# Performance work log

Hardware: AMD Instinct MI355X
Metric: run time of the kernel (lower is better)

## Reference

```python
import jax, jax.numpy as jnp
import numpy as np

B, S, D = 8, 2048, 1024
NEG_INF = jnp.float32(-1e30)  # stand-in for -inf; rows with all-masked are overwritten anyway


def setup_inputs() -> dict:
    key = jax.random.key(0)
    ks = jax.random.split(key, 10)
    query = jax.random.normal(ks[0], (B, S, D), dtype=jnp.float32)
    key_t = jax.random.normal(ks[1], (B, S, D), dtype=jnp.float32)
    value = jax.random.normal(ks[2], (B, S, D), dtype=jnp.float32)
    # pad mask: prefix of valid tokens per batch element (realistic ragged batch)
    lengths = jax.random.randint(ks[3], (B,), S // 2, S + 1)
    pad_masks = jnp.arange(S)[None, :] < lengths[:, None]  # (B, S) bool
    # causal mask, same lower-triangular pattern per batch element
    causal = jnp.tril(jnp.ones((S, S), dtype=bool))
    causal_masks = jnp.broadcast_to(causal, (B, S, S))
    # Linear params (torch nn.Linear: y = x @ W.T + b)
    scale = 0.02
    Wq = jax.random.normal(ks[4], (D, D), dtype=jnp.float32) * scale
    bq = jnp.zeros((D,), dtype=jnp.float32)
    Wk = jax.random.normal(ks[5], (D, D), dtype=jnp.float32) * scale
    bk = jnp.zeros((D,), dtype=jnp.float32)
    Wv = jax.random.normal(ks[6], (D, D), dtype=jnp.float32) * scale
    bv = jnp.zeros((D,), dtype=jnp.float32)
    return {"query": query, "key": key_t, "value": value,
            "pad_masks": pad_masks, "causal_masks": causal_masks,
            "Wq": Wq, "bq": bq, "Wk": Wk, "bk": bk, "Wv": Wv, "bv": bv}


def reference(query, key, value, pad_masks, causal_masks, Wq, bq, Wk, bk, Wv, bv):
    d_model = query.shape[-1]
    Q = jnp.einsum('bsd,ed->bse', query, Wq) + bq
    K = jnp.einsum('bsd,ed->bse', key, Wk) + bk
    V = jnp.einsum('bsd,ed->bse', value, Wv) + bv
    scores = jnp.einsum('bqd,bkd->bqk', Q, K) / jnp.sqrt(jnp.float32(d_model))
    combined = pad_masks[:, None, :] & causal_masks              # (B, S, S)
    row_any = jnp.any(combined, axis=-1, keepdims=True)          # (B, S, 1)
    scores = jnp.where(combined, scores, NEG_INF)
    scores = jnp.where(row_any, scores, jnp.zeros_like(scores))
    attn = jax.nn.softmax(scores, axis=-1)
    attn = jnp.where(row_any, attn, jnp.zeros_like(attn))
    # multiply by pad mask along the QUERY axis (faithful to the torch transpose)
    attn = attn * pad_masks[:, :, None].astype(attn.dtype)
    seq_emds = jnp.einsum('bqk,bkd->bqd', attn, V)
    return seq_emds, attn
```

## Files before the change

### kernel.cpp

```cpp
#include <hip/hip_runtime.h>
#include <hip/hip_bf16.h>

#define B_ 8
#define S_ 2048
#define D_ 1024
#define SCALE 0.03125f

typedef __attribute__((ext_vector_type(4))) float f32x4;
typedef __attribute__((ext_vector_type(8))) short short8;
typedef __attribute__((ext_vector_type(4))) short short4v;

static __device__ inline unsigned short f2bf(float f) {
    unsigned int u = __float_as_uint(f);
    u += 0x7FFF + ((u >> 16) & 1);
    return (unsigned short)(u >> 16);
}

static __device__ __forceinline__ void gload16(const void* g, void* l) {
    __builtin_amdgcn_global_load_lds(
        (const __attribute__((address_space(1))) unsigned int*)g,
        (__attribute__((address_space(3))) unsigned int*)l, 16, 0, 0);
}

static __device__ __forceinline__ void pipe_sync() {
    asm volatile("s_waitcnt vmcnt(0)" ::: "memory");
    __builtin_amdgcn_s_barrier();
    __builtin_amdgcn_sched_barrier(0);
}

static __device__ __forceinline__ int xcd_swz(int hw, int nwg) {
    return (hw & 7) * (nwg >> 3) + (hw >> 3);
}

__global__ void lengths_kernel(const unsigned char* __restrict__ pm, int* __restrict__ lens) {
    __shared__ int cnt[B_];
    int tid = threadIdx.x;
    if (tid < B_) cnt[tid] = 0;
    __syncthreads();
    int layout;
    if (pm[0] == 1 && pm[1] == 1) layout = 0;
    else if (pm[0] == 1) layout = 1;
    else layout = 2;
    for (int i = tid; i < B_ * S_; i += blockDim.x) {
        bool v;
        if (layout == 0) v = pm[i] != 0;
        else if (layout == 1) v = ((const int*)pm)[i] != 0;
        else v = ((const float*)pm)[i] != 0.0f;
        if (v) atomicAdd(&cnt[i >> 11], 1);
    }
    __syncthreads();
    if (tid < B_) lens[tid] = cnt[tid];
}

__global__ void convert_all_kernel(const float* __restrict__ q, const float* __restrict__ k,
                                   const float* __restrict__ v,
                                   const float* __restrict__ Wq, const float* __restrict__ Wk,
                                   const float* __restrict__ Wv,
                                   unsigned short* __restrict__ Xb,
                                   unsigned short* __restrict__ Wb) {
    const int z = blockIdx.z;
    const float* src;
    unsigned short* dst;
    int n;
    if (z < 3) {
        src = (z == 0) ? q : (z == 1) ? k : v;
        dst = Xb + (size_t)z * B_ * S_ * D_;
        n = B_ * S_ * D_;
    } else {
        src = (z == 3) ? Wq : (z == 4) ? Wk : Wv;
        dst = Wb + (size_t)(z - 3) * D_ * D_;
        n = D_ * D_;
    }
    int idx = (blockIdx.x * 256 + threadIdx.x) * 8;
    if (idx >= n) return;
    float4 a = *(const float4*)(src + idx);
    float4 b = *(const float4*)(src + idx + 4);
    short8 o;
    o[0] = (short)f2bf(a.x); o[1] = (short)f2bf(a.y);
    o[2] = (short)f2bf(a.z); o[3] = (short)f2bf(a.w);
    o[4] = (short)f2bf(b.x); o[5] = (short)f2bf(b.y);
    o[6] = (short)f2bf(b.z); o[7] = (short)f2bf(b.w);
    *(short8*)(dst + idx) = o;
}

__global__ void proj_bf16_kernel(const unsigned short* __restrict__ Xb3,
                                 const unsigned short* __restrict__ Wb3,
                                 const float* __restrict__ bq, const float* __restrict__ bk,
                                 const float* __restrict__ bv,
                                 unsigned short* __restrict__ Qb,
                                 unsigned short* __restrict__ Kb,
                                 unsigned short* __restrict__ Vt) {
    const int log_id = xcd_swz(blockIdx.x, 3 * (B_ * S_ / 128) * (D_ / 128));
    const int z = log_id >> 10;
    const int rem = log_id & 1023;
    const int m0 = (rem >> 3) * 128;
    const int n0 = (rem & 7) * 128;

    const unsigned short* Xb = Xb3 + (size_t)z * B_ * S_ * D_;
    const unsigned short* Wb = Wb3 + (size_t)z * D_ * D_;
    const float* bias = (z == 0) ? bq : (z == 1) ? bk : bv;

    __shared__ unsigned short As[2][128 * 32];
    __shared__ unsigned short Bs[2][128 * 32];

    const int tid = threadIdx.x;
    const int lane = tid & 63, w = tid >> 6;
    const int wr = w >> 1, wc = w & 1;
    const int g = lane >> 4, l15 = lane & 15;

    const int flat0 = (w * 2 + 0) * 1024 + lane * 16;
    const int flat1 = (w * 2 + 1) * 1024 + lane * 16;
    const int r0 = flat0 >> 6, cb0 = flat0 & 63;
    const int r1 = flat1 >> 6, cb1 = flat1 & 63;

    auto stage = [&](int buf, int kk) {
        gload16((const char*)Xb + ((size_t)(m0 + r0) * D_ + kk) * 2 + cb0, (char*)&As[buf][0] + flat0);
        gload16((const char*)Xb + ((size_t)(m0 + r1) * D_ + kk) * 2 + cb1, (char*)&As[buf][0] + flat1);
        gload16((const char*)Wb + ((size_t)(n0 + r0) * D_ + kk) * 2 + cb0, (char*)&Bs[buf][0] + flat0);
        gload16((const char*)Wb + ((size_t)(n0 + r1) * D_ + kk) * 2 + cb1, (char*)&Bs[buf][0] + flat1);
    };

    f32x4 acc[4][4];
    const f32x4 z4 = {0.f, 0.f, 0.f, 0.f};
    for (int a = 0; a < 4; ++a)
        for (int b2 = 0; b2 < 4; ++b2) acc[a][b2] = z4;

    stage(0, 0);
    pipe_sync();
    int cur = 0;
    for (int kk = 0; kk < D_; kk += 32) {
        if (kk + 32 < D_) stage(cur ^ 1, kk + 32);
        short8 a_frag[4], b_frag[4];
#pragma unroll
        for (int mf = 0; mf < 4; ++mf)
            a_frag[mf] = *(const short8*)(&As[cur][(wr * 64 + mf * 16 + l15) * 32 + g * 8]);
#pragma unroll
        for (int nf = 0; nf < 4; ++nf)
            b_frag[nf] = *(const short8*)(&Bs[cur][(wc * 64 + nf * 16 + l15) * 32 + g * 8]);
        __builtin_amdgcn_s_setprio(1);
#pragma unroll
        for (int mf = 0; mf < 4; ++mf)
#pragma unroll
            for (int nf = 0; nf < 4; ++nf)
                acc[mf][nf] = __builtin_amdgcn_mfma_f32_16x16x32_bf16(a_frag[mf], b_frag[nf], acc[mf][nf], 0, 0, 0);
        __builtin_amdgcn_s_setprio(0);
        pipe_sync();
        cur ^= 1;
    }

    if (z < 2) {
        unsigned short* O = (z == 0) ? Qb : Kb;
#pragma unroll
        for (int mf = 0; mf < 4; ++mf) {
#pragma unroll
            for (int nf = 0; nf < 4; ++nf) {
                int gm = m0 + wr * 64 + mf * 16 + 4 * g;
                int gn = n0 + wc * 64 + nf * 16 + l15;
                float bb = bias[gn];
#pragma unroll
                for (int i = 0; i < 4; ++i)
                    O[(size_t)(gm + i) * D_ + gn] = f2bf(acc[mf][nf][i] + bb);
            }
        }
    } else {
#pragma unroll
        for (int mf = 0; mf < 4; ++mf) {
#pragma unroll
            for (int nf = 0; nf < 4; ++nf) {
                int gm = m0 + wr * 64 + mf * 16 + 4 * g;
                int b = gm >> 11, tok = gm & 2047;
                int gn = n0 + wc * 64 + nf * 16 + l15;
                float bb = bias[gn];
                short4v sv;
#pragma unroll
                for (int i = 0; i < 4; ++i) sv[i] = (short)f2bf(acc[mf][nf][i] + bb);
                *(short4v*)(&Vt[((size_t)b * D_ + gn) * S_ + tok]) = sv;
            }
        }
    }
}

__global__ void proj_kernel(const float* __restrict__ q, const float* __restrict__ k,
                            const float* __restrict__ v,
                            const float* __restrict__ Wq, const float* __restrict__ Wk,
                            const float* __restrict__ Wv,
                            const float* __restrict__ bq, const float* __restrict__ bk,
                            const float* __restrict__ bv,
                            unsigned short* __restrict__ Qb, unsigned short* __restrict__ Kb,
                            unsigned short* __restrict__ Vt) {
    const int z = blockIdx.z;
    const float* X = (z == 0) ? q : (z == 1) ? k : v;
    const float* W = (z == 0) ? Wq : (z == 1) ? Wk : Wv;
    const float* bias = (z == 0) ? bq : (z == 1) ? bk : bv;

    __shared__ short As[128 * 40];
    __shared__ short Bs[128 * 40];

    const int m0 = blockIdx.y * 128;
    const int n0 = blockIdx.x * 128;
    const int tid = threadIdx.x;
    const int lane = tid & 63, wid = tid >> 6;
    const int wr = wid >> 1, wc = wid & 1;
    const int g = lane >> 4, l15 = lane & 15;

    f32x4 acc[4][4];
    const f32x4 z4 = {0.f, 0.f, 0.f, 0.f};
    for (int a = 0; a < 4; ++a)
        for (int b2 = 0; b2 < 4; ++b2) acc[a][b2] = z4;

    for (int kk = 0; kk < D_; kk += 32) {
#pragma unroll
        for (int it = 0; it < 4; ++it) {
            int flat = it * 1024 + tid * 4;
            int r = flat >> 5, c = flat & 31;
            float4 va = *(const float4*)(X + (size_t)(m0 + r) * D_ + kk + c);
            short4v sa = {(short)f2bf(va.x), (short)f2bf(va.y), (short)f2bf(va.z), (short)f2bf(va.w)};
            *(short4v*)(&As[r * 40 + c]) = sa;
            float4 vb = *(const float4*)(W + (size_t)(n0 + r) * D_ + kk + c);
            short4v sb = {(short)f2bf(vb.x), (short)f2bf(vb.y), (short)f2bf(vb.z), (short)f2bf(vb.w)};
            *(short4v*)(&Bs[r * 40 + c]) = sb;
        }
        __syncthreads();
        short8 a_frag[4], b_frag[4];
#pragma unroll
        for (int mf = 0; mf < 4; ++mf)
            a_frag[mf] = *(const short8*)(&As[(wr * 64 + mf * 16 + l15) * 40 + g * 8]);
#pragma unroll
        for (int nf = 0; nf < 4; ++nf)
            b_frag[nf] = *(const short8*)(&Bs[(wc * 64 + nf * 16 + l15) * 40 + g * 8]);
#pragma unroll
        for (int mf = 0; mf < 4; ++mf)
#pragma unroll
            for (int nf = 0; nf < 4; ++nf)
                acc[mf][nf] = __builtin_amdgcn_mfma_f32_16x16x32_bf16(a_frag[mf], b_frag[nf], acc[mf][nf], 0, 0, 0);
        __syncthreads();
    }

    if (z < 2) {
        unsigned short* O = (z == 0) ? Qb : Kb;
#pragma unroll
        for (int mf = 0; mf < 4; ++mf) {
#pragma unroll
            for (int nf = 0; nf < 4; ++nf) {
                int gm = m0 + wr * 64 + mf * 16 + 4 * g;
                int gn = n0 + wc * 64 + nf * 16 + l15;
                float bb = bias[gn];
#pragma unroll
                for (int i = 0; i < 4; ++i)
                    O[(size_t)(gm + i) * D_ + gn] = f2bf(acc[mf][nf][i] + bb);
            }
        }
    } else {
#pragma unroll
        for (int mf = 0; mf < 4; ++mf) {
#pragma unroll
            for (int nf = 0; nf < 4; ++nf) {
                int gm = m0 + wr * 64 + mf * 16 + 4 * g;
                int b = gm >> 11, tok = gm & 2047;
                int gn = n0 + wc * 64 + nf * 16 + l15;
                float bb = bias[gn];
                short4v sv;
#pragma unroll
                for (int i = 0; i < 4; ++i) sv[i] = (short)f2bf(acc[mf][nf][i] + bb);
                *(short4v*)(&Vt[((size_t)b * D_ + gn) * S_ + tok]) = sv;
            }
        }
    }
}

__global__ void scores_kernel(const unsigned short* __restrict__ Qb,
                              const unsigned short* __restrict__ Kb,
                              const int* __restrict__ lens,
                              float* __restrict__ attn) {
    const int log_id = xcd_swz(blockIdx.x, 136 * B_);
    const int b = log_id / 136;
    const int idx = log_id - b * 136;
    int qt = (int)((sqrtf(8.f * idx + 1.f) - 1.f) * 0.5f);
    while ((qt + 1) * (qt + 2) / 2 <= idx) ++qt;
    while (qt * (qt + 1) / 2 > idx) --qt;
    const int kt = idx - qt * (qt + 1) / 2;
    const int m0 = qt * 128, n0 = kt * 128;
    const int len = lens[b];
    if (m0 >= len) return;

    __shared__ unsigned short As[2][128 * 32];
    __shared__ unsigned short Bs[2][128 * 32];

    const int tid = threadIdx.x;
    const int lane = tid & 63, w = tid >> 6;
    const int wr = w >> 1, wc = w & 1;
    const int g = lane >> 4, l15 = lane & 15;

    const char* Qbase = (const char*)(Qb + (size_t)(b * S_ + m0) * D_);
    const char* Kbase = (const char*)(Kb + (size_t)(b * S_ + n0) * D_);

    const int flat0 = (w * 2 + 0) * 1024 + lane * 16;
    const int flat1 = (w * 2 + 1) * 1024 + lane * 16;
    const int r0 = flat0 >> 6, cb0 = flat0 & 63;
    const int r1 = flat1 >> 6, cb1 = flat1 & 63;

    auto stage = [&](int buf, int kk) {
        gload16(Qbase + (size_t)r0 * (D_ * 2) + kk * 2 + cb0, (char*)&As[buf][0] + flat0);
        gload16(Qbase + (size_t)r1 * (D_ * 2) + kk * 2 + cb1, (char*)&As[buf][0] + flat1);
        gload16(Kbase + (size_t)r0 * (D_ * 2) + kk * 2 + cb0, (char*)&Bs[buf][0] + flat0);
        gload16(Kbase + (size_t)r1 * (D_ * 2) + kk * 2 + cb1, (char*)&Bs[buf][0] + flat1);
    };

    f32x4 acc[4][4];
    const f32x4 z4 = {0.f, 0.f, 0.f, 0.f};
    for (int a = 0; a < 4; ++a)
        for (int b2 = 0; b2 < 4; ++b2) acc[a][b2] = z4;

    stage(0, 0);
    pipe_sync();
    int cur = 0;
    for (int kk = 0; kk < D_; kk += 32) {
        if (kk + 32 < D_) stage(cur ^ 1, kk + 32);
        short8 a_frag[4], b_frag[4];
#pragma unroll
        for (int mf = 0; mf < 4; ++mf)
            a_frag[mf] = *(const short8*)(&As[cur][(wr * 64 + mf * 16 + l15) * 32 + g * 8]);
#pragma unroll
        for (int nf = 0; nf < 4; ++nf)
            b_frag[nf] = *(const short8*)(&Bs[cur][(wc * 64 + nf * 16 + l15) * 32 + g * 8]);
        __builtin_amdgcn_s_setprio(1);
#pragma unroll
        for (int mf = 0; mf < 4; ++mf)
#pragma unroll
            for (int nf = 0; nf < 4; ++nf)
                acc[mf][nf] = __builtin_amdgcn_mfma_f32_16x16x32_bf16(a_frag[mf], b_frag[nf], acc[mf][nf], 0, 0, 0);
        __builtin_amdgcn_s_setprio(0);
        pipe_sync();
        cur ^= 1;
    }

    const bool interior = (m0 >= n0 + 128) && (m0 + 128 <= len);
    if (interior) {
#pragma unroll
        for (int mf = 0; mf < 4; ++mf) {
#pragma unroll
            for (int nf = 0; nf < 4; ++nf) {
                int gm = m0 + wr * 64 + mf * 16 + 4 * g;
                int gn = n0 + wc * 64 + nf * 16 + l15;
#pragma unroll
                for (int i = 0; i < 4; ++i)
                    attn[(size_t)(b * S_ + gm + i) * S_ + gn] = acc[mf][nf][i] * SCALE;
            }
        }
    } else {
#pragma unroll
        for (int mf = 0; mf < 4; ++mf) {
#pragma unroll
            for (int nf = 0; nf < 4; ++nf) {
                int gm = m0 + wr * 64 + mf * 16 + 4 * g;
                int gn = n0 + wc * 64 + nf * 16 + l15;
#pragma unroll
                for (int i = 0; i < 4; ++i) {
                    int rq = gm + i;
                    if (rq < len && gn <= rq)
                        attn[(size_t)(b * S_ + rq) * S_ + gn] = acc[mf][nf][i] * SCALE;
                }
            }
        }
    }
}

__global__ void softmax_kernel(const int* __restrict__ lens,
                               float* __restrict__ attn, unsigned short* __restrict__ P) {
    const int row = blockIdx.x;
    const int b = row >> 11, qpos = row & 2047;
    const int tid = threadIdx.x;
    const size_t rbase = (size_t)row * S_;
    const int c0 = tid * 8;
    const short8 zp = {0, 0, 0, 0, 0, 0, 0, 0};
    const float4 zf = {0.f, 0.f, 0.f, 0.f};
    if (qpos >= lens[b]) {
        *(short8*)(&P[rbase + c0]) = zp;
        *(float4*)(attn + rbase + c0) = zf;
        *(float4*)(attn + rbase + c0 + 4) = zf;
        return;
    }
    __shared__ float wm[4], wl[4];
    const bool act = (c0 <= qpos);
    float x[8];
    if (act) {
        float4 a0 = *(const float4*)(attn + rbase + c0);
        float4 a1 = *(const float4*)(attn + rbase + c0 + 4);
        x[0] = a0.x; x[1] = a0.y; x[2] = a0.z; x[3] = a0.w;
        x[4] = a1.x; x[5] = a1.y; x[6] = a1.z; x[7] = a1.w;
#pragma unroll
        for (int j = 0; j < 8; ++j)
            if (c0 + j > qpos) x[j] = -1e30f;
    } else {
#pragma unroll
        for (int j = 0; j < 8; ++j) x[j] = -1e30f;
    }
    float lmax = -1e30f;
#pragma unroll
    for (int j = 0; j < 8; ++j) lmax = fmaxf(lmax, x[j]);
#pragma unroll
    for (int off = 1; off < 64; off <<= 1) lmax = fmaxf(lmax, __shfl_xor(lmax, off));
    if ((tid & 63) == 0) wm[tid >> 6] = lmax;
    __syncthreads();
    const float m = fmaxf(fmaxf(wm[0], wm[1]), fmaxf(wm[2], wm[3]));
    float e[8];
    float lsum = 0.f;
#pragma unroll
    for (int j = 0; j < 8; ++j) {
        e[j] = (x[j] > -1e29f) ? __expf(x[j] - m) : 0.f;
        lsum += e[j];
    }
#pragma unroll
    for (int off = 1; off < 64; off <<= 1) lsum += __shfl_xor(lsum, off);
    if ((tid & 63) == 0) wl[tid >> 6] = lsum;
    __syncthreads();
    if (act) {
        const float inv = 1.0f / (wl[0] + wl[1] + wl[2] + wl[3]);
        float4 o0, o1;
        short8 pb;
#pragma unroll
        for (int j = 0; j < 8; ++j) {
            e[j] *= inv;
            pb[j] = (short)f2bf(e[j]);
        }
        o0.x = e[0]; o0.y = e[1]; o0.z = e[2]; o0.w = e[3];
        o1.x = e[4]; o1.y = e[5]; o1.z = e[6]; o1.w = e[7];
        *(float4*)(attn + rbase + c0) = o0;
        *(float4*)(attn + rbase + c0 + 4) = o1;
        *(short8*)(&P[rbase + c0]) = pb;
    } else {
        *(float4*)(attn + rbase + c0) = zf;
        *(float4*)(attn + rbase + c0 + 4) = zf;
        *(short8*)(&P[rbase + c0]) = zp;
    }
}

__global__ void pv_kernel(const unsigned short* __restrict__ P,
                          const unsigned short* __restrict__ Vt,
                          const int* __restrict__ lens, float* __restrict__ seq) {
    const int log_id = xcd_swz(blockIdx.x, B_ * (S_ / 128) * (D_ / 128));
    const int b = log_id >> 7;
    const int rem = log_id & 127;
    const int q0 = (rem >> 3) * 128;
    const int n0 = (rem & 7) * 128;
    const int len = lens[b];
    const int tid = threadIdx.x;

    if (q0 >= len) {
        const float4 zf = {0.f, 0.f, 0.f, 0.f};
#pragma unroll
        for (int it = 0; it < 16; ++it) {
            int flat = it * 1024 + tid * 4;
            int r = flat >> 7, c = flat & 127;
            *(float4*)(&seq[(size_t)(b * S_ + q0 + r) * D_ + n0 + c]) = zf;
        }
        return;
    }

    __shared__ unsigned short As[2][128 * 32];
    __shared__ unsigned short Bs[2][128 * 32];
    const int lane = tid & 63, w = tid >> 6;
    const int wr = w >> 1, wc = w & 1;
    const int g = lane >> 4, l15 = lane & 15;

    const char* Pbase = (const char*)(P + (size_t)(b * S_ + q0) * S_);
    const char* Vbase = (const char*)(Vt + ((size_t)b * D_ + n0) * S_);

    const int flat0 = (w * 2 + 0) * 1024 + lane * 16;
    const int flat1 = (w * 2 + 1) * 1024 + lane * 16;
    const int r0 = flat0 >> 6, cb0 = flat0 & 63;
    const int r1 = flat1 >> 6, cb1 = flat1 & 63;

    auto stage = [&](int buf, int k0) {
        gload16(Pbase + (size_t)r0 * (S_ * 2) + k0 * 2 + cb0, (char*)&As[buf][0] + flat0);
        gload16(Pbase + (size_t)r1 * (S_ * 2) + k0 * 2 + cb1, (char*)&As[buf][0] + flat1);
        gload16(Vbase + (size_t)r0 * (S_ * 2) + k0 * 2 + cb0, (char*)&Bs[buf][0] + flat0);
        gload16(Vbase + (size_t)r1 * (S_ * 2) + k0 * 2 + cb1, (char*)&Bs[buf][0] + flat1);
    };

    f32x4 acc[4][4];
    const f32x4 z4 = {0.f, 0.f, 0.f, 0.f};
    for (int a = 0; a < 4; ++a)
        for (int b2 = 0; b2 < 4; ++b2) acc[a][b2] = z4;

    const int nkt = (q0 + 128) / 32;

    stage(0, 0);
    pipe_sync();
    int cur = 0;
    for (int kt = 0; kt < nkt; ++kt) {
        if (kt + 1 < nkt) stage(cur ^ 1, (kt + 1) * 32);
        short8 a_frag[4], b_frag[4];
#pragma unroll
        for (int mf = 0; mf < 4; ++mf)
            a_frag[mf] = *(const short8*)(&As[cur][(wr * 64 + mf * 16 + l15) * 32 + g * 8]);
#pragma unroll
        for (int nf = 0; nf < 4; ++nf)
            b_frag[nf] = *(const short8*)(&Bs[cur][(wc * 64 + nf * 16 + l15) * 32 + g * 8]);
        __builtin_amdgcn_s_setprio(1);
#pragma unroll
        for (int mf = 0; mf < 4; ++mf)
#pragma unroll
            for (int nf = 0; nf < 4; ++nf)
                acc[mf][nf] = __builtin_amdgcn_mfma_f32_16x16x32_bf16(a_frag[mf], b_frag[nf], acc[mf][nf], 0, 0, 0);
        __builtin_amdgcn_s_setprio(0);
        pipe_sync();
        cur ^= 1;
    }

#pragma unroll
    for (int mf = 0; mf < 4; ++mf) {
#pragma unroll
        for (int nf = 0; nf < 4; ++nf) {
            int gq = q0 + wr * 64 + mf * 16 + 4 * g;
            int gn = n0 + wc * 64 + nf * 16 + l15;
#pragma unroll
            for (int i = 0; i < 4; ++i)
                seq[(size_t)(b * S_ + gq + i) * D_ + gn] = acc[mf][nf][i];
        }
    }
}

extern "C" void kernel_launch(void* const* d_in, const int* in_sizes, int n_in,
                              void* d_out, int out_size, void* d_ws, size_t ws_size,
                              hipStream_t stream) {
    const float* q = (const float*)d_in[0];
    const float* k = (const float*)d_in[1];
    const float* v = (const float*)d_in[2];
    const unsigned char* pm = (const unsigned char*)d_in[3];
    const float* Wq = (const float*)d_in[5];
    const float* bq = (const float*)d_in[6];
    const float* Wk = (const float*)d_in[7];
    const float* bk = (const float*)d_in[8];
    const float* Wv = (const float*)d_in[9];
    const float* bv = (const float*)d_in[10];

    float* seq = (float*)d_out;
    float* attn = seq + (size_t)B_ * S_ * D_;

    char* ws = (char*)d_ws;
    int* lens = (int*)ws;
    unsigned short* Qb = (unsigned short*)(ws + 256);
    unsigned short* Kb = Qb + (size_t)B_ * S_ * D_;
    unsigned short* Vt = Kb + (size_t)B_ * S_ * D_;
    unsigned short* Xb = Vt + (size_t)B_ * D_ * S_;
    unsigned short* Wb = Xb + 3ull * B_ * S_ * D_;
    unsigned short* P = Qb;

    const size_t need = 256 + 6ull * B_ * S_ * D_ * 2 + 3ull * D_ * D_ * 2;

    lengths_kernel<<<1, 256, 0, stream>>>(pm, lens);

    if (ws_size >= need) {
        convert_all_kernel<<<dim3(B_ * S_ * D_ / 2048, 1, 6), 256, 0, stream>>>(
            q, k, v, Wq, Wk, Wv, Xb, Wb);
        proj_bf16_kernel<<<dim3(3 * (B_ * S_ / 128) * (D_ / 128)), 256, 0, stream>>>(
            Xb, Wb, bq, bk, bv, Qb, Kb, Vt);
    } else {
        proj_kernel<<<dim3(D_ / 128, (B_ * S_) / 128, 3), 256, 0, stream>>>(
            q, k, v, Wq, Wk, Wv, bq, bk, bv, Qb, Kb, Vt);
    }

    scores_kernel<<<dim3(136 * B_), 256, 0, stream>>>(Qb, Kb, lens, attn);
    softmax_kernel<<<dim3(B_ * S_), 256, 0, stream>>>(lens, attn, P);
    pv_kernel<<<dim3(B_ * (S_ / 128) * (D_ / 128)), 256, 0, stream>>>(P, Vt, lens, seq);
}
```

Before: 405.2 us.

## Rewrite QKV projection GEMM with 256x256 tiles, 512 threads, swizzled LDS

Replaces the 128x128, 256-thread projection GEMM with a 256x256-tile kernel using 8 waves, a K-step of 64, and an XOR-swizzled LDS layout to avoid bank conflicts. Each wave now computes a 128x64 sub-tile in two halves, reusing its B fragments, with the next tile's global-to-LDS loads issued during compute. The goal is higher arithmetic intensity and better MFMA utilization for the projection stage. The cost is more registers, 128KB of LDS limiting occupancy to one block, and extra barriers per k-step.

```diff
diff --git a/kernel.cpp b/kernel.cpp
--- a/kernel.cpp
+++ b/kernel.cpp
@@ -5,6 +5,7 @@
 #define S_ 2048
 #define D_ 1024
 #define SCALE 0.03125f
+#define NT_ (D_ / 64)
 
 typedef __attribute__((ext_vector_type(4))) float f32x4;
 typedef __attribute__((ext_vector_type(8))) short short8;
@@ -30,6 +31,10 @@
 
 static __device__ __forceinline__ int xcd_swz(int hw, int nwg) {
     return (hw & 7) * (nwg >> 3) + (hw >> 3);
+}
+
+static __device__ __forceinline__ int swz(int byte) {
+    return byte ^ (((byte >> 9) & 1) << 5);
 }
 
 __global__ void lengths_kernel(const unsigned char* __restrict__ pm, int* __restrict__ lens) {
@@ -83,79 +88,118 @@
     *(short8*)(dst + idx) = o;
 }
 
-__global__ void proj_bf16_kernel(const unsigned short* __restrict__ Xb3,
-                                 const unsigned short* __restrict__ Wb3,
-                                 const float* __restrict__ bq, const float* __restrict__ bk,
-                                 const float* __restrict__ bv,
-                                 unsigned short* __restrict__ Qb,
-                                 unsigned short* __restrict__ Kb,
-                                 unsigned short* __restrict__ Vt) {
-    const int log_id = xcd_swz(blockIdx.x, 3 * (B_ * S_ / 128) * (D_ / 128));
-    const int z = log_id >> 10;
-    const int rem = log_id & 1023;
-    const int m0 = (rem >> 3) * 128;
-    const int n0 = (rem & 7) * 128;
+__global__ __launch_bounds__(512, 1) void proj2_kernel(
+        const unsigned short* __restrict__ Xb3,
+        const unsigned short* __restrict__ Wb3,
+        const float* __restrict__ bq, const float* __restrict__ bk,
+        const float* __restrict__ bv,
+        unsigned short* __restrict__ Qb,
+        unsigned short* __restrict__ Kb,
+        unsigned short* __restrict__ Vt) {
+    const int nwg = 3 * (B_ * S_ / 256) * (D_ / 256);
+    const int log_id = xcd_swz(blockIdx.x, nwg);
+    const int z = log_id >> 8;
+    const int rem = log_id & 255;
+    const int m0 = (rem >> 2) * 256;
+    const int n0 = (rem & 3) * 256;
 
     const unsigned short* Xb = Xb3 + (size_t)z * B_ * S_ * D_;
     const unsigned short* Wb = Wb3 + (size_t)z * D_ * D_;
     const float* bias = (z == 0) ? bq : (z == 1) ? bk : bv;
 
-    __shared__ unsigned short As[2][128 * 32];
-    __shared__ unsigned short Bs[2][128 * 32];
+    __shared__ unsigned short lds[2][2][2][128 * 64];
 
     const int tid = threadIdx.x;
-    const int lane = tid & 63, w = tid >> 6;
-    const int wr = w >> 1, wc = w & 1;
+    const int lane = tid & 63, wid = tid >> 6;
+    const int wm = wid >> 2, wn = wid & 3;
     const int g = lane >> 4, l15 = lane & 15;
 
-    const int flat0 = (w * 2 + 0) * 1024 + lane * 16;
-    const int flat1 = (w * 2 + 1) * 1024 + lane * 16;
-    const int r0 = flat0 >> 6, cb0 = flat0 & 63;
-    const int r1 = flat1 >> 6, cb1 = flat1 & 63;
-
-    auto stage = [&](int buf, int kk) {
-        gload16((const char*)Xb + ((size_t)(m0 + r0) * D_ + kk) * 2 + cb0, (char*)&As[buf][0] + flat0);
-        gload16((const char*)Xb + ((size_t)(m0 + r1) * D_ + kk) * 2 + cb1, (char*)&As[buf][0] + flat1);
-        gload16((const char*)Wb + ((size_t)(n0 + r0) * D_ + kk) * 2 + cb0, (char*)&Bs[buf][0] + flat0);
-        gload16((const char*)Wb + ((size_t)(n0 + r1) * D_ + kk) * 2 + cb1, (char*)&Bs[buf][0] + flat1);
+    const int f0 = tid * 16;
+    const int r0s = f0 >> 7, c0s = f0 & 127;
+    const int csrc = c0s ^ (((r0s >> 2) & 1) << 5);
+
+    f32x4 acc[8][4];
+    const f32x4 z4 = {0.f, 0.f, 0.f, 0.f};
+#pragma unroll
+    for (int a = 0; a < 8; ++a)
+#pragma unroll
+        for (int b2 = 0; b2 < 4; ++b2) acc[a][b2] = z4;
+
+    auto stageT = [&](int buf, int kk) {
+#pragma unroll
+        for (int h = 0; h < 2; ++h) {
+            gload16((const char*)Xb + ((size_t)(m0 + h * 128 + r0s) * D_ + kk) * 2 + csrc,
+                    (char*)&lds[buf][0][h][0] + f0);
+            gload16((const char*)Xb + ((size_t)(m0 + h * 128 + r0s + 64) * D_ + kk) * 2 + csrc,
+                    (char*)&lds[buf][0][h][0] + f0 + 8192);
+            gload16((const char*)Wb + ((size_t)(n0 + h * 128 + r0s) * D_ + kk) * 2 + csrc,
+                    (char*)&lds[buf][1][h][0] + f0);
+            gload16((const char*)Wb + ((size_t)(n0 + h * 128 + r0s + 64) * D_ + kk) * 2 + csrc,
+                    (char*)&lds[buf][1][h][0] + f0 + 8192);
+        }
     };
 
-    f32x4 acc[4][4];
-    const f32x4 z4 = {0.f, 0.f, 0.f, 0.f};
-    for (int a = 0; a < 4; ++a)
-        for (int b2 = 0; b2 < 4; ++b2) acc[a][b2] = z4;
-
-    stage(0, 0);
+    stageT(0, 0);
     pipe_sync();
-    int cur = 0;
-    for (int kk = 0; kk < D_; kk += 32) {
-        if (kk + 32 < D_) stage(cur ^ 1, kk + 32);
-        short8 a_frag[4], b_frag[4];
-#pragma unroll
-        for (int mf = 0; mf < 4; ++mf)
-            a_frag[mf] = *(const short8*)(&As[cur][(wr * 64 + mf * 16 + l15) * 32 + g * 8]);
-#pragma unroll
-        for (int nf = 0; nf < 4; ++nf)
-            b_frag[nf] = *(const short8*)(&Bs[cur][(wc * 64 + nf * 16 + l15) * 32 + g * 8]);
-        __builtin_amdgcn_s_setprio(1);
-#pragma unroll
-        for (int mf = 0; mf < 4; ++mf)
-#pragma unroll
-            for (int nf = 0; nf < 4; ++nf)
-                acc[mf][nf] = __builtin_amdgcn_mfma_f32_16x16x32_bf16(a_frag[mf], b_frag[nf], acc[mf][nf], 0, 0, 0);
-        __builtin_amdgcn_s_setprio(0);
-        pipe_sync();
-        cur ^= 1;
+
+    for (int T = 0; T < NT_; ++T) {
+        const int buf = T & 1;
+        const char* Abase = (const char*)&lds[buf][0][wm][0];
+        short8 afr[4], bfr[4];
+#pragma unroll
+        for (int ks = 0; ks < 2; ++ks) {
+            const int colb = ks * 64 + g * 16;
+            if (ks == 0 && T + 1 < NT_) stageT(buf ^ 1, (T + 1) * 64);
+#pragma unroll
+            for (int nf = 0; nf < 4; ++nf) {
+                int nl = wn * 64 + nf * 16 + l15;
+                bfr[nf] = *(const short8*)((const char*)&lds[buf][1][nl >> 7][0]
+                                           + swz((nl & 127) * 128 + colb));
+            }
+#pragma unroll
+            for (int mf = 0; mf < 4; ++mf)
+                afr[mf] = *(const short8*)(Abase + swz((mf * 16 + l15) * 128 + colb));
+            __builtin_amdgcn_s_barrier();
+            asm volatile("s_waitcnt lgkmcnt(0)" ::: "memory");
+            __builtin_amdgcn_sched_barrier(0);
+            __builtin_amdgcn_s_setprio(1);
+#pragma unroll
+            for (int mf = 0; mf < 4; ++mf)
+#pragma unroll
+                for (int nf = 0; nf < 4; ++nf)
+                    acc[mf][nf] = __builtin_amdgcn_mfma_f32_16x16x32_bf16(
+                        afr[mf], bfr[nf], acc[mf][nf], 0, 0, 0);
+            __builtin_amdgcn_s_setprio(0);
+            __builtin_amdgcn_s_barrier();
+#pragma unroll
+            for (int mf = 0; mf < 4; ++mf)
+                afr[mf] = *(const short8*)(Abase + swz(((mf + 4) * 16 + l15) * 128 + colb));
+            __builtin_amdgcn_s_barrier();
+            asm volatile("s_waitcnt lgkmcnt(0)" ::: "memory");
+            __builtin_amdgcn_sched_barrier(0);
+            __builtin_amdgcn_s_setprio(1);
+#pragma unroll
+            for (int mf = 0; mf < 4; ++mf)
+#pragma unroll
+                for (int nf = 0; nf < 4; ++nf)
+                    acc[mf + 4][nf] = __builtin_amdgcn_mfma_f32_16x16x32_bf16(
+                        afr[mf], bfr[nf], acc[mf + 4][nf], 0, 0, 0);
+            __builtin_amdgcn_s_setprio(0);
+            __builtin_amdgcn_s_barrier();
+        }
+        if (T + 1 < NT_) asm volatile("s_waitcnt vmcnt(0)" ::: "memory");
+        __builtin_amdgcn_s_barrier();
+        __builtin_amdgcn_sched_barrier(0);
     }
 
     if (z < 2) {
         unsigned short* O = (z == 0) ? Qb : Kb;
 #pragma unroll
-        for (int mf = 0; mf < 4; ++mf) {
+        for (int mf = 0; mf < 8; ++mf) {
 #pragma unroll
             for (int nf = 0; nf < 4; ++nf) {
-                int gm = m0 + wr * 64 + mf * 16 + 4 * g;
-                int gn = n0 + wc * 64 + nf * 16 + l15;
+                int gm = m0 + wm * 128 + mf * 16 + 4 * g;
+                int gn = n0 + wn * 64 + nf * 16 + l15;
                 float bb = bias[gn];
 #pragma unroll
                 for (int i = 0; i < 4; ++i)
@@ -164,12 +208,12 @@
         }
     } else {
 #pragma unroll
-        for (int mf = 0; mf < 4; ++mf) {
+        for (int mf = 0; mf < 8; ++mf) {
 #pragma unroll
             for (int nf = 0; nf < 4; ++nf) {
-                int gm = m0 + wr * 64 + mf * 16 + 4 * g;
+                int gm = m0 + wm * 128 + mf * 16 + 4 * g;
                 int b = gm >> 11, tok = gm & 2047;
-                int gn = n0 + wc * 64 + nf * 16 + l15;
+                int gn = n0 + wn * 64 + nf * 16 + l15;
                 float bb = bias[gn];
                 short4v sv;
 #pragma unroll
@@ -554,7 +598,7 @@
     if (ws_size >= need) {
         convert_all_kernel<<<dim3(B_ * S_ * D_ / 2048, 1, 6), 256, 0, stream>>>(
             q, k, v, Wq, Wk, Wv, Xb, Wb);
-        proj_bf16_kernel<<<dim3(3 * (B_ * S_ / 128) * (D_ / 128)), 256, 0, stream>>>(
+        proj2_kernel<<<dim3(3 * (B_ * S_ / 256) * (D_ / 256)), 512, 0, stream>>>(
             Xb, Wb, bq, bk, bv, Qb, Kb, Vt);
     } else {
         proj_kernel<<<dim3(D_ / 128, (B_ * S_) / 128, 3), 256, 0, stream>>>(
```

Result: no change. 408.7 us (+0.9%).
